# Optimization experiments

Hardware: AMD Instinct MI355X
Metric: run time of the kernel (lower is better)

The kernel has to match this reference:

```python
import jax, jax.numpy as jnp
import numpy as np
from jax import lax

DIM = 64
HEADS = 8
B, H, W = 4, 256, 256


def layer_norm(x, w, b):
    # WithBias LayerNorm over channel dim (dim=1 of NCHW), per-pixel
    mu = jnp.mean(x, axis=1, keepdims=True)
    var = jnp.mean((x - mu) ** 2, axis=1, keepdims=True)
    xn = (x - mu) / jnp.sqrt(var + 1e-5)
    return xn * w[None, :, None, None] + b[None, :, None, None]


def conv1x1(x, w, b=None):
    out = jnp.einsum('oc,bchw->bohw', w, x)
    if b is not None:
        out = out + b[None, :, None, None]
    return out


def dwconv3x3(x, w):
    # w: [C,1,3,3], depthwise (groups=C), stride 1, pad 1
    return lax.conv_general_dilated(
        x, w, window_strides=(1, 1), padding=((1, 1), (1, 1)),
        feature_group_count=x.shape[1],
        dimension_numbers=('NCHW', 'OIHW', 'NCHW'))


def modulation(v, y, mw, mb):
    # mw: [4, C, C] = [scale0, scale1, shift0, shift1]; mb: [4, C]
    s = conv1x1(jax.nn.leaky_relu(conv1x1(y, mw[0], mb[0]), 0.1), mw[1], mb[1])
    t = conv1x1(jax.nn.leaky_relu(conv1x1(y, mw[2], mb[2]), 0.1), mw[3], mb[3])
    return v * (s + 1.0) + t


def _heads(t):
    b, c, h, w = t.shape
    return t.reshape(b, HEADS, c // HEADS, h * w)


def channel_attn(q, k, v, temp):
    b, c, h, w = v.shape
    q, k, v = _heads(q), _heads(k), _heads(v)  # b, head, ch, hw
    q = q / jnp.maximum(jnp.linalg.norm(q, axis=-1, keepdims=True), 1e-12)
    k = k / jnp.maximum(jnp.linalg.norm(k, axis=-1, keepdims=True), 1e-12)
    attn = jnp.einsum('bhcn,bhdn->bhcd', q, k) * temp[None]  # small CxC
    attn = jax.nn.softmax(attn, axis=-1)
    out = jnp.einsum('bhcd,bhdn->bhcn', attn, v)
    return out.reshape(b, c, h, w)


def setup_inputs() -> dict:
    key = jax.random.key(0)
    ks = jax.random.split(key, 24)
    sc = 0.05
    d = {
        'x': jax.random.normal(ks[0], (B, DIM, H, W), jnp.float32),
        'y': jax.random.normal(ks[1], (B, DIM, H, W), jnp.float32),
        'ln_w': jnp.ones((DIM,), jnp.float32),
        'ln_b': jnp.zeros((DIM,), jnp.float32),
        'temp': jnp.ones((HEADS, 1, 1), jnp.float32),
        'kv1_w': jax.random.normal(ks[2], (2 * DIM, DIM), jnp.float32) * sc,
        'kvdw1_w': jax.random.normal(ks[3], (2 * DIM, 1, 3, 3), jnp.float32) * sc,
        'q1_w': jax.random.normal(ks[4], (DIM, DIM), jnp.float32) * sc,
        'qdw1_w': jax.random.normal(ks[5], (DIM, 1, 3, 3), jnp.float32) * sc,
        'po1_w': jax.random.normal(ks[6], (DIM, DIM), jnp.float32) * sc,
        'kv2_w': jax.random.normal(ks[7], (2 * DIM, DIM), jnp.float32) * sc,
        'kvdw2_w': jax.random.normal(ks[8], (2 * DIM, 1, 3, 3), jnp.float32) * sc,
        'q2_w': jax.random.normal(ks[9], (DIM, DIM), jnp.float32) * sc,
        'qdw2_w': jax.random.normal(ks[10], (DIM, 1, 3, 3), jnp.float32) * sc,
        'po2_w': jax.random.normal(ks[11], (DIM, DIM), jnp.float32) * sc,
        'mm1_w': jax.random.normal(ks[12], (4, DIM, DIM), jnp.float32) * sc,
        'mm1_b': jnp.zeros((4, DIM), jnp.float32),
        'mm2_w': jax.random.normal(ks[13], (4, DIM, DIM), jnp.float32) * sc,
        'mm2_b': jnp.zeros((4, DIM), jnp.float32),
    }
    return d


def reference(x, y, ln_w, ln_b, temp,
              kv1_w, kvdw1_w, q1_w, qdw1_w, po1_w,
              kv2_w, kvdw2_w, q2_w, qdw2_w, po2_w,
              mm1_w, mm1_b, mm2_w, mm2_b):
    x1 = layer_norm(x, ln_w, ln_b)
    y1 = layer_norm(y, ln_w, ln_b)  # original reuses self.norm1 for both

    # branch 1: kv from x1, q from y1, v modulated by x, residual y
    kv1 = dwconv3x3(conv1x1(x1, kv1_w), kvdw1_w)
    k1, v1 = jnp.split(kv1, 2, axis=1)
    q1 = dwconv3x3(conv1x1(y1, q1_w), qdw1_w)
    v1 = modulation(v1, x, mm1_w, mm1_b)
    out1 = conv1x1(channel_attn(q1, k1, v1, temp), po1_w) + y

    # branch 2: kv from y1, q from x1, v modulated by y, residual x
    kv2 = dwconv3x3(conv1x1(y1, kv2_w), kvdw2_w)
    k2, v2 = jnp.split(kv2, 2, axis=1)
    q2 = dwconv3x3(conv1x1(x1, q2_w), qdw2_w)
    v2 = modulation(v2, y, mm2_w, mm2_b)
    out2 = conv1x1(channel_attn(q2, k2, v2, temp), po2_w) + x

    return (out1, out2)
```

## Files before the change

### kernel.cpp

```cpp
#include <hip/hip_runtime.h>
#include <hip/hip_bf16.h>

#define HW 65536
#define BATCH 4
#define NPIX (BATCH*HW)

typedef unsigned short u16;
typedef unsigned int   u32;
typedef __attribute__((ext_vector_type(8))) short bh8;
typedef __attribute__((ext_vector_type(4))) float f4;

__device__ __forceinline__ float b2f(u16 u){
    u32 i = ((u32)u) << 16; float f; __builtin_memcpy(&f, &i, 4); return f;
}
__device__ __forceinline__ u16 f2b(float f){
    __hip_bfloat16 h = __float2bfloat16(f); u16 u; __builtin_memcpy(&u, &h, 2); return u;
}

__device__ __forceinline__ f4 mfma16(bh8 a, bh8 b, f4 c){
    return __builtin_amdgcn_mfma_f32_16x16x32_bf16(a, b, c, 0, 0, 0);
}

struct CvtJob { const float* src; u16* dst; int n; const float* cs; };
struct SetupArgs {
    CvtJob j[12];
    const float* kvw[2]; const float* qw[2];
    const float* lnw; const float* lnb;
    float* sums; float* lnc;
};
__global__ __launch_bounds__(256) void setup_kernel(SetupArgs S){
    int blk = blockIdx.x;
    if (blk < 12){
        const CvtJob J = S.j[blk];
        if (J.cs){
            for (int i = threadIdx.x; i < J.n; i += 256) J.dst[i] = f2b(J.src[i] * J.cs[i & 63]);
        } else {
            for (int i = threadIdx.x; i < J.n; i += 256) J.dst[i] = f2b(J.src[i]);
        }
        return;
    }
    int pb = blk - 12;
    if (pb == 0){
        for (int i = threadIdx.x; i < 5120; i += 256) S.sums[i] = 0.f;
    } else {
        int seg = pb - 1;
        int o = threadIdx.x;
        if (o < 192){
            const float* W = (o < 128) ? S.kvw[seg] : S.qw[1-seg];
            int row = (o < 128) ? o : o - 128;
            float a = 0.f, bb = 0.f;
            for (int c = 0; c < 64; c++){
                float wv = W[row*64 + c];
                a = fmaf(wv, S.lnw[c], a); bb = fmaf(wv, S.lnb[c], bb);
            }
            S.lnc[seg*384 + o] = a; S.lnc[seg*384 + 192 + o] = bb;
        }
    }
}

struct GemmMerged {
    const float* in[2];
    const u16* wa[2];
    const float* rs[2]; const float* rb[2];
    u16* out0[2]; u16* out1[2]; u16* out2[2];
};
__global__ __launch_bounds__(256) void gemmln_kernel(GemmMerged G){
    __shared__ u16 wl[192*64];
    int seg = blockIdx.x >> 10, tile = blockIdx.x & 1023;
    int w = threadIdx.x >> 6, lane = threadIdx.x & 63;
    int quad = lane >> 4, l16 = lane & 15;
    int b = tile >> 8;
    int pbase = ((tile & 255) << 8) + (w << 6) + (l16 << 2);

    const float* in = G.in[seg];
    f4 fin[8], fin2[8];
    #pragma unroll
    for (int j = 0; j < 8; j++)
        fin[j] = *(const f4*)(in + ((size_t)b*64 + quad*8 + j)*HW + pbase);
    #pragma unroll
    for (int j = 0; j < 8; j++)
        fin2[j] = *(const f4*)(in + ((size_t)b*64 + 32 + quad*8 + j)*HW + pbase);

    {
        const u16* W = G.wa[seg];
        for (int i = threadIdx.x; i < 192*8; i += 256){
            int row = i >> 3, ch = i & 7;
            uint4 v = *(const uint4*)(W + row*64 + ch*8);
            *(uint4*)(wl + row*64 + ((ch ^ (row & 7)) << 3)) = v;
        }
    }
    __syncthreads();

    float s1[4] = {0.f,0.f,0.f,0.f}, s2[4] = {0.f,0.f,0.f,0.f};
    bh8 bfr[2][4];
    #pragma unroll
    for (int j = 0; j < 8; j++){
        f4 fv = fin[j];
        #pragma unroll
        for (int p = 0; p < 4; p++){
            float v = fv[p];
            s1[p] += v; s2[p] = fmaf(v, v, s2[p]);
            bfr[0][p][j] = (short)f2b(v);
        }
    }
    #pragma unroll
    for (int j = 0; j < 8; j++){
        f4 fv = fin2[j];
        #pragma unroll
        for (int p = 0; p < 4; p++){
            float v = fv[p];
            s1[p] += v; s2[p] = fmaf(v, v, s2[p]);
            bfr[1][p][j] = (short)f2b(v);
        }
    }

    float mu[4], iv[4];
    #pragma unroll
    for (int p = 0; p < 4; p++){
        s1[p] += __shfl_xor(s1[p], 16); s1[p] += __shfl_xor(s1[p], 32);
        s2[p] += __shfl_xor(s2[p], 16); s2[p] += __shfl_xor(s2[p], 32);
        mu[p] = s1[p]*(1.f/64.f);
        iv[p] = rsqrtf(s2[p]*(1.f/64.f) - mu[p]*mu[p] + 1e-5f);
    }

    const float* rs = G.rs[seg]; const float* rb = G.rb[seg];
    u16* o0 = G.out0[seg]; u16* o1 = G.out1[seg]; u16* o2 = G.out2[seg];
    #pragma unroll
    for (int mi = 0; mi < 12; mi++){
        f4 acc[4];
        #pragma unroll
        for (int p = 0; p < 4; p++) acc[p] = (f4){0.f,0.f,0.f,0.f};
        #pragma unroll
        for (int ks = 0; ks < 2; ks++){
            bh8 a;
            __builtin_memcpy(&a, wl + (mi*16 + l16)*64 + ((((ks<<2)+quad) ^ (l16 & 7)) << 3), 16);
            #pragma unroll
            for (int p = 0; p < 4; p++)
                acc[p] = mfma16(a, bfr[ks][p], acc[p]);
        }
        u16* dst = (mi < 4) ? o0 : (mi < 8) ? o1 : o2;
        #pragma unroll
        for (int r = 0; r < 4; r++){
            int o = mi*16 + quad*4 + r;
            size_t pidx = ((size_t)b*64 + (o & 63))*HW + pbase;
            float rsv = rs[o], rbv = rb[o];
            float v0 = iv[0]*(acc[0][r] - mu[0]*rsv) + rbv;
            float v1 = iv[1]*(acc[1][r] - mu[1]*rsv) + rbv;
            float v2 = iv[2]*(acc[2][r] - mu[2]*rsv) + rbv;
            float v3 = iv[3]*(acc[3][r] - mu[3]*rsv) + rbv;
            uint2 st;
            st.x = (u32)f2b(v0) | ((u32)f2b(v1) << 16);
            st.y = (u32)f2b(v2) | ((u32)f2b(v3) << 16);
            *(uint2*)(dst + pidx) = st;
        }
    }
}

struct Dw6 { const u16* in[6]; u16* out[6]; const float* w[6]; int choff[6]; };
__global__ __launch_bounds__(256) void dw6_kernel(Dw6 A){
    int seg = blockIdx.x >> 13;
    int lid = ((blockIdx.x & 8191) << 8) + threadIdx.x;
    const u16* inp = A.in[seg];
    u16* outp      = A.out[seg];
    const float* wd = A.w[seg];
    int choff      = A.choff[seg];
    int bc = lid >> 13;
    int n8 = lid & 8191;
    int h = n8 >> 5, c8 = (n8 & 31) << 3;
    const float* wc = wd + ((size_t)((bc & 63) + choff))*9;
    const u16* p = inp + (size_t)bc*HW;
    float row[3][10];
    #pragma unroll
    for (int r = 0; r < 3; r++){
        int hh = h - 1 + r;
        bool ok = (unsigned)hh < 256u;
        const u16* pr = p + hh*256 + c8;
        if (ok){
            uint4 m = *(const uint4*)pr;
            row[r][1] = b2f((u16)m.x); row[r][2] = b2f((u16)(m.x>>16));
            row[r][3] = b2f((u16)m.y); row[r][4] = b2f((u16)(m.y>>16));
            row[r][5] = b2f((u16)m.z); row[r][6] = b2f((u16)(m.z>>16));
            row[r][7] = b2f((u16)m.w); row[r][8] = b2f((u16)(m.w>>16));
        } else {
            #pragma unroll
            for (int j = 1; j < 9; j++) row[r][j] = 0.f;
        }
        float lft = __shfl_up(row[r][8], 1);
        float rgt = __shfl_down(row[r][1], 1);
        row[r][0] = (c8 > 0)   ? lft : 0.f;
        row[r][9] = (c8 < 248) ? rgt : 0.f;
    }
    float o[8];
    #pragma unroll
    for (int i = 0; i < 8; i++){
        float a = 0.f;
        #pragma unroll
        for (int r = 0; r < 3; r++){
            a = fmaf(wc[r*3+0], row[r][i],   a);
            a = fmaf(wc[r*3+1], row[r][i+1], a);
            a = fmaf(wc[r*3+2], row[r][i+2], a);
        }
        o[i] = a;
    }
    uint4 st;
    st.x = (u32)f2b(o[0]) | ((u32)f2b(o[1])<<16);
    st.y = (u32)f2b(o[2]) | ((u32)f2b(o[3])<<16);
    st.z = (u32)f2b(o[4]) | ((u32)f2b(o[5])<<16);
    st.w = (u32)f2b(o[6]) | ((u32)f2b(o[7])<<16);
    *(uint4*)(outp + (size_t)bc*HW + h*256 + c8) = st;
}

#define NSL 64
struct AttnDual { const u16* q[2]; const u16* k[2]; float* sums; };
__global__ __launch_bounds__(256) void attn_part_kernel(AttnDual AD){
    int seg = blockIdx.x >> 11;
    int blk = blockIdx.x & 2047;
    int sl = blk & (NSL-1);
    int bh = blk >> 6;
    int b = bh >> 3, h = bh & 7;
    const u16* qp = AD.q[seg] + ((size_t)b*64 + h*8)*HW + sl*(HW/NSL);
    const u16* kp = AD.k[seg] + ((size_t)b*64 + h*8)*HW + sl*(HW/NSL);
    float acc[80];
    #pragma unroll
    for (int i = 0; i < 80; i++) acc[i] = 0.f;
    int n0 = threadIdx.x << 2;
    float qv[8][4], kw[8][4];
    #pragma unroll
    for (int i = 0; i < 8; i++){
        uint2 mq = *(const uint2*)(qp + (size_t)i*HW + n0);
        uint2 mk = *(const uint2*)(kp + (size_t)i*HW + n0);
        qv[i][0] = b2f((u16)(mq.x & 0xffffu)); qv[i][1] = b2f((u16)(mq.x >> 16));
        qv[i][2] = b2f((u16)(mq.y & 0xffffu)); qv[i][3] = b2f((u16)(mq.y >> 16));
        kw[i][0] = b2f((u16)(mk.x & 0xffffu)); kw[i][1] = b2f((u16)(mk.x >> 16));
        kw[i][2] = b2f((u16)(mk.y & 0xffffu)); kw[i][3] = b2f((u16)(mk.y >> 16));
    }
    #pragma unroll
    for (int i = 0; i < 8; i++){
        #pragma unroll
        for (int u = 0; u < 4; u++){
            acc[64+i] = fmaf(qv[i][u], qv[i][u], acc[64+i]);
            acc[72+i] = fmaf(kw[i][u], kw[i][u], acc[72+i]);
        }
        #pragma unroll
        for (int j = 0; j < 8; j++)
            #pragma unroll
            for (int u = 0; u < 4; u++)
                acc[i*8+j] = fmaf(qv[i][u], kw[j][u], acc[i*8+j]);
    }
    __shared__ float sred[4][80];
    int lane = threadIdx.x & 63, wv = threadIdx.x >> 6;
    #pragma unroll
    for (int t = 0; t < 80; t++){
        float r = acc[t];
        r += __shfl_down(r, 32); r += __shfl_down(r, 16); r += __shfl_down(r, 8);
        r += __shfl_down(r, 4);  r += __shfl_down(r, 2);  r += __shfl_down(r, 1);
        if (lane == 0) sred[wv][t] = r;
    }
    __syncthreads();
    if (threadIdx.x < 80){
        int t = threadIdx.x;
        atomicAdd(&AD.sums[seg*2560 + bh*80 + t], sred[0][t]+sred[1][t]+sred[2][t]+sred[3][t]);
    }
}

struct WeffDual { const float* sums; const float* temp; const float* po[2]; u16* weff[2]; };
__global__ __launch_bounds__(64) void weff_kernel(WeffDual WD){
    int seg = blockIdx.x >> 2;
    int b = blockIdx.x & 3;
    const float* po = WD.po[seg];
    u16* weff = WD.weff[seg];
    __shared__ float at[8][8][8];
    int t = threadIdx.x;
    {
        int h = t >> 3, i = t & 7;
        const float* f = WD.sums + seg*2560 + (b*8 + h)*80;
        float iq = 1.f / fmaxf(sqrtf(f[64+i]), 1e-12f);
        float tv = WD.temp[h];
        float row[8]; float m = -1e30f;
        #pragma unroll
        for (int j = 0; j < 8; j++){
            float ik = 1.f / fmaxf(sqrtf(f[72+j]), 1e-12f);
            row[j] = f[i*8+j]*iq*ik*tv;
            m = fmaxf(m, row[j]);
        }
        float s = 0.f;
        #pragma unroll
        for (int j = 0; j < 8; j++){ row[j] = expf(row[j]-m); s += row[j]; }
        float rsv = 1.f/s;
        #pragma unroll
        for (int j = 0; j < 8; j++) at[h][i][j] = row[j]*rsv;
    }
    __syncthreads();
    int o = t;
    for (int g = 0; g < 64; g++){
        int h = g >> 3, j = g & 7;
        float wv = 0.f;
        #pragma unroll
        for (int i = 0; i < 8; i++) wv = fmaf(po[o*64 + h*8 + i], at[h][i][j], wv);
        weff[b*4096 + o*64 + g] = f2b(wv);
    }
}

struct ModFinal {
    const float* in[2]; const u16* wa[2]; const u16* wb[2];
    const float* b0[2]; const float* b2[2]; const float* b1[2]; const float* b3[2];
    const u16* wf[2];
    const u16* v[2];
    const float* resid[2];
    float* out[2];
};
__global__ __launch_bounds__(256) void modfinal_kernel(ModFinal M){
    __shared__ u32 lds[128*128];
    int seg = blockIdx.x >> 10, tile = blockIdx.x & 1023;
    int w = threadIdx.x >> 6, lane = threadIdx.x & 63;
    int quad = lane >> 4, l16 = lane & 15;
    int b = tile >> 8;
    int pbase = ((tile & 255) << 8) + (w << 6) + (l16 << 2);
    int pp = ((w << 4) + l16) << 1;

    const float* in = M.in[seg];
    const u16* wa = M.wa[seg];

    f4 fin[8], fin2[8];
    #pragma unroll
    for (int j = 0; j < 8; j++)
        fin[j] = *(const f4*)(in + ((size_t)b*64 + quad*8 + j)*HW + pbase);
    #pragma unroll
    for (int j = 0; j < 8; j++)
        fin2[j] = *(const f4*)(in + ((size_t)b*64 + 32 + quad*8 + j)*HW + pbase);

    f4 acc[8][4];
    #pragma unroll
    for (int mi = 0; mi < 8; mi++)
        #pragma unroll
        for (int p = 0; p < 4; p++) acc[mi][p] = (f4){0.f,0.f,0.f,0.f};

    #pragma unroll
    for (int ks = 0; ks < 2; ks++){
        bh8 bfr[4];
        #pragma unroll
        for (int j = 0; j < 8; j++){
            f4 fv = (ks == 0) ? fin[j] : fin2[j];
            #pragma unroll
            for (int p = 0; p < 4; p++) bfr[p][j] = (short)f2b(fv[p]);
        }
        #pragma unroll
        for (int mi = 0; mi < 8; mi++){
            bh8 a;
            __builtin_memcpy(&a, wa + (mi*16 + l16)*64 + ks*32 + quad*8, 16);
            #pragma unroll
            for (int p = 0; p < 4; p++)
                acc[mi][p] = mfma16(a, bfr[p], acc[mi][p]);
        }
    }

    uint2 vpref[16];
    {
        const u16* vP = M.v[seg];
        #pragma unroll
        for (int mi = 0; mi < 4; mi++)
        #pragma unroll
        for (int r = 0; r < 4; r++)
            vpref[mi*4+r] = *(const uint2*)(vP + ((size_t)b*64 + mi*16 + quad*4 + r)*HW + pbase);
    }

    {
        const float* b0v = M.b0[seg]; const float* b2v = M.b2[seg];
        #pragma unroll
        for (int mi = 0; mi < 8; mi++)
        #pragma unroll
        for (int r = 0; r < 4; r++){
            int o = mi*16 + quad*4 + r;
            float bi = (o < 64) ? b0v[o] : b2v[o-64];
            float v0 = acc[mi][0][r] + bi; v0 = v0 > 0.f ? v0 : 0.1f*v0;
            float v1 = acc[mi][1][r] + bi; v1 = v1 > 0.f ? v1 : 0.1f*v1;
            float v2 = acc[mi][2][r] + bi; v2 = v2 > 0.f ? v2 : 0.1f*v2;
            float v3 = acc[mi][3][r] + bi; v3 = v3 > 0.f ? v3 : 0.1f*v3;
            uint2 st;
            st.x = (u32)f2b(v0) | ((u32)f2b(v1) << 16);
            st.y = (u32)f2b(v2) | ((u32)f2b(v3) << 16);
            *(uint2*)&lds[o*128 + ((pp + ((o>>2)&3)*8) & 127)] = st;
        }
    }
    __syncthreads();

    const u16* wb = M.wb[seg];
    f4 acc2[8][4];
    #pragma unroll
    for (int mi = 0; mi < 8; mi++)
        #pragma unroll
        for (int p = 0; p < 4; p++) acc2[mi][p] = (f4){0.f,0.f,0.f,0.f};
    #pragma unroll
    for (int ks = 0; ks < 4; ks++){
        int kb = ks*32 + quad*8;
        bh8 bfr[4];
        #pragma unroll
        for (int j = 0; j < 8; j++){
            int ch = kb + j;
            uint2 m = *(const uint2*)&lds[ch*128 + ((pp + ((ch>>2)&3)*8) & 127)];
            bfr[0][j] = (short)(m.x & 0xffffu);
            bfr[1][j] = (short)(m.x >> 16);
            bfr[2][j] = (short)(m.y & 0xffffu);
            bfr[3][j] = (short)(m.y >> 16);
        }
        #pragma unroll
        for (int mi = 0; mi < 8; mi++){
            if (mi < 4 ? (ks < 2) : (ks >= 2)){
                int ksl = (mi >= 4) ? ks - 2 : ks;
                bh8 a;
                __builtin_memcpy(&a, wb + (mi*16 + l16)*64 + ksl*32 + quad*8, 16);
                #pragma unroll
                for (int p = 0; p < 4; p++)
                    acc2[mi][p] = mfma16(a, bfr[p], acc2[mi][p]);
            }
        }
    }
    __syncthreads();

    {
        const float* b1v = M.b1[seg]; const float* b3v = M.b3[seg];
        #pragma unroll
        for (int mi = 0; mi < 4; mi++)
        #pragma unroll
        for (int r = 0; r < 4; r++){
            int o = mi*16 + quad*4 + r;
            uint2 vv = vpref[mi*4+r];
            float va[4] = { b2f((u16)(vv.x & 0xffffu)), b2f((u16)(vv.x >> 16)),
                            b2f((u16)(vv.y & 0xffffu)), b2f((u16)(vv.y >> 16)) };
            float ov[4];
            #pragma unroll
            for (int p = 0; p < 4; p++){
                float s = acc2[mi][p][r] + b1v[o];
                float t = acc2[mi+4][p][r] + b3v[o];
                ov[p] = va[p]*(s+1.f)+t;
            }
            uint2 st;
            st.x = (u32)f2b(ov[0]) | ((u32)f2b(ov[1]) << 16);
            st.y = (u32)f2b(ov[2]) | ((u32)f2b(ov[3]) << 16);
            *(uint2*)&lds[o*128 + ((pp + ((o>>2)&3)*8) & 127)] = st;
        }
    }
    f4 rpre[16];
    {
        const float* resid = M.resid[seg];
        #pragma unroll
        for (int mi = 0; mi < 4; mi++)
        #pragma unroll
        for (int r = 0; r < 4; r++)
            rpre[mi*4+r] = *(const f4*)(resid + ((size_t)b*64 + mi*16 + quad*4 + r)*HW + pbase);
    }
    __syncthreads();

    const u16* wf = M.wf[seg] + b*4096;
    f4 accF[4][4];
    #pragma unroll
    for (int mi = 0; mi < 4; mi++)
        #pragma unroll
        for (int p = 0; p < 4; p++) accF[mi][p] = (f4){0.f,0.f,0.f,0.f};
    #pragma unroll
    for (int ks = 0; ks < 2; ks++){
        int kb = ks*32 + quad*8;
        bh8 bfr[4];
        #pragma unroll
        for (int j = 0; j < 8; j++){
            int ch = kb + j;
            uint2 m = *(const uint2*)&lds[ch*128 + ((pp + ((ch>>2)&3)*8) & 127)];
            bfr[0][j] = (short)(m.x & 0xffffu);
            bfr[1][j] = (short)(m.x >> 16);
            bfr[2][j] = (short)(m.y & 0xffffu);
            bfr[3][j] = (short)(m.y >> 16);
        }
        #pragma unroll
        for (int mi = 0; mi < 4; mi++){
            bh8 a;
            __builtin_memcpy(&a, wf + (mi*16 + l16)*64 + ks*32 + quad*8, 16);
            #pragma unroll
            for (int p = 0; p < 4; p++)
                accF[mi][p] = mfma16(a, bfr[p], accF[mi][p]);
        }
    }
    {
        float* outF = M.out[seg];
        #pragma unroll
        for (int mi = 0; mi < 4; mi++)
        #pragma unroll
        for (int r = 0; r < 4; r++){
            int o = mi*16 + quad*4 + r;
            size_t pidx = ((size_t)b*64 + o)*HW + pbase;
            f4 rr = rpre[mi*4+r];
            f4 st;
            #pragma unroll
            for (int p = 0; p < 4; p++) st[p] = accF[mi][p][r] + rr[p];
            *(f4*)(outF + pidx) = st;
        }
    }
}

extern "C" void kernel_launch(void* const* d_in, const int* in_sizes, int n_in,
                              void* d_out, int out_size, void* d_ws, size_t ws_size,
                              hipStream_t stream){
    const float* x    = (const float*)d_in[0];
    const float* y    = (const float*)d_in[1];
    const float* ln_w = (const float*)d_in[2];
    const float* ln_b = (const float*)d_in[3];
    const float* temp = (const float*)d_in[4];
    const float* kv_w[2]   = {(const float*)d_in[5],  (const float*)d_in[10]};
    const float* kvdw_w[2] = {(const float*)d_in[6],  (const float*)d_in[11]};
    const float* q_w[2]    = {(const float*)d_in[7],  (const float*)d_in[12]};
    const float* qdw_w[2]  = {(const float*)d_in[8],  (const float*)d_in[13]};
    const float* po_w[2]   = {(const float*)d_in[9],  (const float*)d_in[14]};
    const float* mm_w[2]   = {(const float*)d_in[15], (const float*)d_in[17]};
    const float* mm_b[2]   = {(const float*)d_in[16], (const float*)d_in[18]};

    const size_t HPE = (size_t)BATCH*64*HW;
    u16* PL = (u16*)d_ws;
    u16* P[12];
    for (int i = 0; i < 12; i++) P[i] = PL + (size_t)i*HPE;
    float* sums = (float*)(PL + 12*HPE);
    float* lnc  = sums + 5120;
    u16* warena = (u16*)(lnc + 768);
    const int WG[2] = {0, 12288};
    const int WMA[2] = {24576, 40960}, WMB[2] = {32768, 49152};
    const int WEFF[2] = {57344, 73728};

    size_t need = 12*HPE*2 + (5120+768)*4 + 90112*2;
    if (ws_size < need) return;

    SetupArgs S{};
    int nj = 0;
    auto add = [&](const float* s, u16* d, int n, const float* cs){ S.j[nj] = {s, d, n, cs}; nj++; };
    add(kv_w[0], warena + WG[0],        8192, ln_w);
    add(q_w[1],  warena + WG[0] + 8192, 4096, ln_w);
    add(kv_w[1], warena + WG[1],        8192, ln_w);
    add(q_w[0],  warena + WG[1] + 8192, 4096, ln_w);
    for (int br = 0; br < 2; br++){
        add(mm_w[br],        warena + WMA[br],        4096, nullptr);
        add(mm_w[br]+8192,   warena + WMA[br] + 4096, 4096, nullptr);
        add(mm_w[br]+4096,   warena + WMB[br],        4096, nullptr);
        add(mm_w[br]+12288,  warena + WMB[br] + 4096, 4096, nullptr);
    }
    S.kvw[0] = kv_w[0]; S.kvw[1] = kv_w[1];
    S.qw[0]  = q_w[0];  S.qw[1]  = q_w[1];
    S.lnw = ln_w; S.lnb = ln_b; S.sums = sums; S.lnc = lnc;
    setup_kernel<<<15, 256, 0, stream>>>(S);

    const int GT = NPIX/256;

    GemmMerged GK{};
    GK.in[0] = x; GK.in[1] = y;
    GK.wa[0] = warena + WG[0]; GK.wa[1] = warena + WG[1];
    GK.rs[0] = lnc;        GK.rb[0] = lnc + 192;
    GK.rs[1] = lnc + 384;  GK.rb[1] = lnc + 576;
    GK.out0[0] = P[0]; GK.out1[0] = P[1]; GK.out2[0] = P[5];
    GK.out0[1] = P[2]; GK.out1[1] = P[3]; GK.out2[1] = P[4];
    gemmln_kernel<<<2*GT, 256, 0, stream>>>(GK);

    Dw6 D{};
    D.in[0] = P[0];  D.out[0] = P[6];  D.w[0] = kvdw_w[0]; D.choff[0] = 0;
    D.in[1] = P[1];  D.out[1] = P[7];  D.w[1] = kvdw_w[0]; D.choff[1] = 64;
    D.in[2] = P[4];  D.out[2] = P[8];  D.w[2] = qdw_w[0];  D.choff[2] = 0;
    D.in[3] = P[2];  D.out[3] = P[9];  D.w[3] = kvdw_w[1]; D.choff[3] = 0;
    D.in[4] = P[3];  D.out[4] = P[10]; D.w[4] = kvdw_w[1]; D.choff[4] = 64;
    D.in[5] = P[5];  D.out[5] = P[11]; D.w[5] = qdw_w[1];  D.choff[5] = 0;
    dw6_kernel<<<6*8192, 256, 0, stream>>>(D);

    AttnDual AD{};
    AD.q[0] = P[8];  AD.k[0] = P[6];
    AD.q[1] = P[11]; AD.k[1] = P[9];
    AD.sums = sums;
    attn_part_kernel<<<2*BATCH*8*NSL, 256, 0, stream>>>(AD);

    WeffDual WD{};
    WD.sums = sums; WD.temp = temp;
    WD.po[0] = po_w[0]; WD.po[1] = po_w[1];
    WD.weff[0] = warena + WEFF[0]; WD.weff[1] = warena + WEFF[1];
    weff_kernel<<<2*BATCH, 64, 0, stream>>>(WD);

    float* outp = (float*)d_out;
    ModFinal M{};
    M.in[0] = x; M.in[1] = y;
    M.wa[0] = warena + WMA[0]; M.wa[1] = warena + WMA[1];
    M.wb[0] = warena + WMB[0]; M.wb[1] = warena + WMB[1];
    M.b0[0] = mm_b[0];       M.b0[1] = mm_b[1];
    M.b2[0] = mm_b[0] + 128; M.b2[1] = mm_b[1] + 128;
    M.b1[0] = mm_b[0] + 64;  M.b1[1] = mm_b[1] + 64;
    M.b3[0] = mm_b[0] + 192; M.b3[1] = mm_b[1] + 192;
    M.wf[0] = warena + WEFF[0]; M.wf[1] = warena + WEFF[1];
    M.v[0] = P[7]; M.v[1] = P[10];
    M.resid[0] = y; M.resid[1] = x;
    M.out[0] = outp; M.out[1] = outp + HPE;
    modfinal_kernel<<<2*GT, 256, 0, stream>>>(M);
}
```

Before: 611.7 us.

## Restructure modulation kernel to halve LDS and cut register pressure for occupancy

The modulation+final kernel is reordered to process the scale and shift MLP branches one after the other, each through a 64-channel LDS staging area, instead of holding all 128 hidden channels in accumulators and LDS at once. LDS per block drops from 64KB to 32KB and launch bounds request 4 blocks per CU, so more waves can be resident to hide global memory latency. The price is extra LDS round-trips and barriers, the intermediate scale values are now kept packed as bf16 in registers, and capping registers may cause spills.

```diff
diff --git a/kernel.cpp b/kernel.cpp
--- a/kernel.cpp
+++ b/kernel.cpp
@@ -309,8 +309,8 @@
     const float* resid[2];
     float* out[2];
 };
-__global__ __launch_bounds__(256) void modfinal_kernel(ModFinal M){
-    __shared__ u32 lds[128*128];
+__global__ __launch_bounds__(256,4) void modfinal_kernel(ModFinal M){
+    __shared__ u32 lds[64*128];
     int seg = blockIdx.x >> 10, tile = blockIdx.x & 1023;
     int w = threadIdx.x >> 6, lane = threadIdx.x & 63;
     int quad = lane >> 4, l16 = lane & 15;
@@ -320,178 +320,241 @@
 
     const float* in = M.in[seg];
     const u16* wa = M.wa[seg];
-
-    f4 fin[8], fin2[8];
-    #pragma unroll
-    for (int j = 0; j < 8; j++)
-        fin[j] = *(const f4*)(in + ((size_t)b*64 + quad*8 + j)*HW + pbase);
-    #pragma unroll
-    for (int j = 0; j < 8; j++)
-        fin2[j] = *(const f4*)(in + ((size_t)b*64 + 32 + quad*8 + j)*HW + pbase);
-
-    f4 acc[8][4];
-    #pragma unroll
-    for (int mi = 0; mi < 8; mi++)
-        #pragma unroll
-        for (int p = 0; p < 4; p++) acc[mi][p] = (f4){0.f,0.f,0.f,0.f};
-
+    const u16* wb = M.wb[seg];
+
+    bh8 bfr[2][4];
+    {
+        f4 fin[8];
+        #pragma unroll
+        for (int j = 0; j < 8; j++)
+            fin[j] = *(const f4*)(in + ((size_t)b*64 + quad*8 + j)*HW + pbase);
+        #pragma unroll
+        for (int j = 0; j < 8; j++)
+            #pragma unroll
+            for (int p = 0; p < 4; p++) bfr[0][p][j] = (short)f2b(fin[j][p]);
+        #pragma unroll
+        for (int j = 0; j < 8; j++)
+            fin[j] = *(const f4*)(in + ((size_t)b*64 + 32 + quad*8 + j)*HW + pbase);
+        #pragma unroll
+        for (int j = 0; j < 8; j++)
+            #pragma unroll
+            for (int p = 0; p < 4; p++) bfr[1][p][j] = (short)f2b(fin[j][p]);
+    }
+
+    {
+        const float* b0v = M.b0[seg];
+        #pragma unroll
+        for (int mi = 0; mi < 4; mi++){
+            f4 acc[4];
+            #pragma unroll
+            for (int p = 0; p < 4; p++) acc[p] = (f4){0.f,0.f,0.f,0.f};
+            #pragma unroll
+            for (int ks = 0; ks < 2; ks++){
+                bh8 a;
+                __builtin_memcpy(&a, wa + (mi*16 + l16)*64 + ks*32 + quad*8, 16);
+                #pragma unroll
+                for (int p = 0; p < 4; p++) acc[p] = mfma16(a, bfr[ks][p], acc[p]);
+            }
+            #pragma unroll
+            for (int r = 0; r < 4; r++){
+                int o = mi*16 + quad*4 + r;
+                float bi = b0v[o];
+                float v0 = acc[0][r] + bi; v0 = v0 > 0.f ? v0 : 0.1f*v0;
+                float v1 = acc[1][r] + bi; v1 = v1 > 0.f ? v1 : 0.1f*v1;
+                float v2 = acc[2][r] + bi; v2 = v2 > 0.f ? v2 : 0.1f*v2;
+                float v3 = acc[3][r] + bi; v3 = v3 > 0.f ? v3 : 0.1f*v3;
+                uint2 st;
+                st.x = (u32)f2b(v0) | ((u32)f2b(v1) << 16);
+                st.y = (u32)f2b(v2) | ((u32)f2b(v3) << 16);
+                *(uint2*)&lds[o*128 + ((pp + ((o>>2)&3)*8) & 127)] = st;
+            }
+        }
+    }
+    __syncthreads();
+
+    bh8 bsr[2][4];
     #pragma unroll
     for (int ks = 0; ks < 2; ks++){
-        bh8 bfr[4];
-        #pragma unroll
-        for (int j = 0; j < 8; j++){
-            f4 fv = (ks == 0) ? fin[j] : fin2[j];
-            #pragma unroll
-            for (int p = 0; p < 4; p++) bfr[p][j] = (short)f2b(fv[p]);
-        }
-        #pragma unroll
-        for (int mi = 0; mi < 8; mi++){
-            bh8 a;
-            __builtin_memcpy(&a, wa + (mi*16 + l16)*64 + ks*32 + quad*8, 16);
-            #pragma unroll
-            for (int p = 0; p < 4; p++)
-                acc[mi][p] = mfma16(a, bfr[p], acc[mi][p]);
-        }
-    }
-
-    uint2 vpref[16];
-    {
-        const u16* vP = M.v[seg];
-        #pragma unroll
-        for (int mi = 0; mi < 4; mi++)
-        #pragma unroll
-        for (int r = 0; r < 4; r++)
-            vpref[mi*4+r] = *(const uint2*)(vP + ((size_t)b*64 + mi*16 + quad*4 + r)*HW + pbase);
-    }
-
-    {
-        const float* b0v = M.b0[seg]; const float* b2v = M.b2[seg];
-        #pragma unroll
-        for (int mi = 0; mi < 8; mi++)
-        #pragma unroll
-        for (int r = 0; r < 4; r++){
-            int o = mi*16 + quad*4 + r;
-            float bi = (o < 64) ? b0v[o] : b2v[o-64];
-            float v0 = acc[mi][0][r] + bi; v0 = v0 > 0.f ? v0 : 0.1f*v0;
-            float v1 = acc[mi][1][r] + bi; v1 = v1 > 0.f ? v1 : 0.1f*v1;
-            float v2 = acc[mi][2][r] + bi; v2 = v2 > 0.f ? v2 : 0.1f*v2;
-            float v3 = acc[mi][3][r] + bi; v3 = v3 > 0.f ? v3 : 0.1f*v3;
-            uint2 st;
-            st.x = (u32)f2b(v0) | ((u32)f2b(v1) << 16);
-            st.y = (u32)f2b(v2) | ((u32)f2b(v3) << 16);
-            *(uint2*)&lds[o*128 + ((pp + ((o>>2)&3)*8) & 127)] = st;
-        }
-    }
-    __syncthreads();
-
-    const u16* wb = M.wb[seg];
-    f4 acc2[8][4];
-    #pragma unroll
-    for (int mi = 0; mi < 8; mi++)
-        #pragma unroll
-        for (int p = 0; p < 4; p++) acc2[mi][p] = (f4){0.f,0.f,0.f,0.f};
-    #pragma unroll
-    for (int ks = 0; ks < 4; ks++){
         int kb = ks*32 + quad*8;
-        bh8 bfr[4];
         #pragma unroll
         for (int j = 0; j < 8; j++){
             int ch = kb + j;
             uint2 m = *(const uint2*)&lds[ch*128 + ((pp + ((ch>>2)&3)*8) & 127)];
-            bfr[0][j] = (short)(m.x & 0xffffu);
-            bfr[1][j] = (short)(m.x >> 16);
-            bfr[2][j] = (short)(m.y & 0xffffu);
-            bfr[3][j] = (short)(m.y >> 16);
-        }
-        #pragma unroll
-        for (int mi = 0; mi < 8; mi++){
-            if (mi < 4 ? (ks < 2) : (ks >= 2)){
-                int ksl = (mi >= 4) ? ks - 2 : ks;
+            bsr[ks][0][j] = (short)(m.x & 0xffffu);
+            bsr[ks][1][j] = (short)(m.x >> 16);
+            bsr[ks][2][j] = (short)(m.y & 0xffffu);
+            bsr[ks][3][j] = (short)(m.y >> 16);
+        }
+    }
+    __syncthreads();
+
+    {
+        const float* b2v = M.b2[seg];
+        #pragma unroll
+        for (int mi = 0; mi < 4; mi++){
+            f4 acc[4];
+            #pragma unroll
+            for (int p = 0; p < 4; p++) acc[p] = (f4){0.f,0.f,0.f,0.f};
+            #pragma unroll
+            for (int ks = 0; ks < 2; ks++){
                 bh8 a;
-                __builtin_memcpy(&a, wb + (mi*16 + l16)*64 + ksl*32 + quad*8, 16);
+                __builtin_memcpy(&a, wa + ((64 + mi*16 + l16))*64 + ks*32 + quad*8, 16);
                 #pragma unroll
-                for (int p = 0; p < 4; p++)
-                    acc2[mi][p] = mfma16(a, bfr[p], acc2[mi][p]);
-            }
-        }
-    }
-    __syncthreads();
-
-    {
-        const float* b1v = M.b1[seg]; const float* b3v = M.b3[seg];
-        #pragma unroll
-        for (int mi = 0; mi < 4; mi++)
-        #pragma unroll
-        for (int r = 0; r < 4; r++){
-            int o = mi*16 + quad*4 + r;
-            uint2 vv = vpref[mi*4+r];
-            float va[4] = { b2f((u16)(vv.x & 0xffffu)), b2f((u16)(vv.x >> 16)),
-                            b2f((u16)(vv.y & 0xffffu)), b2f((u16)(vv.y >> 16)) };
-            float ov[4];
-            #pragma unroll
-            for (int p = 0; p < 4; p++){
-                float s = acc2[mi][p][r] + b1v[o];
-                float t = acc2[mi+4][p][r] + b3v[o];
-                ov[p] = va[p]*(s+1.f)+t;
-            }
-            uint2 st;
-            st.x = (u32)f2b(ov[0]) | ((u32)f2b(ov[1]) << 16);
-            st.y = (u32)f2b(ov[2]) | ((u32)f2b(ov[3]) << 16);
-            *(uint2*)&lds[o*128 + ((pp + ((o>>2)&3)*8) & 127)] = st;
-        }
-    }
-    f4 rpre[16];
-    {
-        const float* resid = M.resid[seg];
-        #pragma unroll
-        for (int mi = 0; mi < 4; mi++)
-        #pragma unroll
-        for (int r = 0; r < 4; r++)
-            rpre[mi*4+r] = *(const f4*)(resid + ((size_t)b*64 + mi*16 + quad*4 + r)*HW + pbase);
-    }
-    __syncthreads();
-
-    const u16* wf = M.wf[seg] + b*4096;
-    f4 accF[4][4];
-    #pragma unroll
-    for (int mi = 0; mi < 4; mi++)
-        #pragma unroll
-        for (int p = 0; p < 4; p++) accF[mi][p] = (f4){0.f,0.f,0.f,0.f};
+                for (int p = 0; p < 4; p++) acc[p] = mfma16(a, bfr[ks][p], acc[p]);
+            }
+            #pragma unroll
+            for (int r = 0; r < 4; r++){
+                int o = mi*16 + quad*4 + r;
+                float bi = b2v[o];
+                float v0 = acc[0][r] + bi; v0 = v0 > 0.f ? v0 : 0.1f*v0;
+                float v1 = acc[1][r] + bi; v1 = v1 > 0.f ? v1 : 0.1f*v1;
+                float v2 = acc[2][r] + bi; v2 = v2 > 0.f ? v2 : 0.1f*v2;
+                float v3 = acc[3][r] + bi; v3 = v3 > 0.f ? v3 : 0.1f*v3;
+                uint2 st;
+                st.x = (u32)f2b(v0) | ((u32)f2b(v1) << 16);
+                st.y = (u32)f2b(v2) | ((u32)f2b(v3) << 16);
+                *(uint2*)&lds[o*128 + ((pp + ((o>>2)&3)*8) & 127)] = st;
+            }
+        }
+    }
+
+    uint2 spk[4][4];
+    {
+        const float* b1v = M.b1[seg];
+        #pragma unroll
+        for (int mi = 0; mi < 4; mi++){
+            f4 acc[4];
+            #pragma unroll
+            for (int p = 0; p < 4; p++) acc[p] = (f4){0.f,0.f,0.f,0.f};
+            #pragma unroll
+            for (int ks = 0; ks < 2; ks++){
+                bh8 a;
+                __builtin_memcpy(&a, wb + (mi*16 + l16)*64 + ks*32 + quad*8, 16);
+                #pragma unroll
+                for (int p = 0; p < 4; p++) acc[p] = mfma16(a, bsr[ks][p], acc[p]);
+            }
+            #pragma unroll
+            for (int r = 0; r < 4; r++){
+                int o = mi*16 + quad*4 + r;
+                float bi = b1v[o];
+                uint2 st;
+                st.x = (u32)f2b(acc[0][r] + bi) | ((u32)f2b(acc[1][r] + bi) << 16);
+                st.y = (u32)f2b(acc[2][r] + bi) | ((u32)f2b(acc[3][r] + bi) << 16);
+                spk[mi][r] = st;
+            }
+        }
+    }
+    __syncthreads();
+
+    bh8 btr[2][4];
     #pragma unroll
     for (int ks = 0; ks < 2; ks++){
         int kb = ks*32 + quad*8;
-        bh8 bfr[4];
         #pragma unroll
         for (int j = 0; j < 8; j++){
             int ch = kb + j;
             uint2 m = *(const uint2*)&lds[ch*128 + ((pp + ((ch>>2)&3)*8) & 127)];
-            bfr[0][j] = (short)(m.x & 0xffffu);
-            bfr[1][j] = (short)(m.x >> 16);
-            bfr[2][j] = (short)(m.y & 0xffffu);
-            bfr[3][j] = (short)(m.y >> 16);
-        }
+            btr[ks][0][j] = (short)(m.x & 0xffffu);
+            btr[ks][1][j] = (short)(m.x >> 16);
+            btr[ks][2][j] = (short)(m.y & 0xffffu);
+            btr[ks][3][j] = (short)(m.y >> 16);
+        }
+    }
+    uint2 vpref[16];
+    {
+        const u16* vP = M.v[seg];
+        #pragma unroll
+        for (int mi = 0; mi < 4; mi++)
+        #pragma unroll
+        for (int r = 0; r < 4; r++)
+            vpref[mi*4+r] = *(const uint2*)(vP + ((size_t)b*64 + mi*16 + quad*4 + r)*HW + pbase);
+    }
+    __syncthreads();
+
+    {
+        const float* b3v = M.b3[seg];
         #pragma unroll
         for (int mi = 0; mi < 4; mi++){
-            bh8 a;
-            __builtin_memcpy(&a, wf + (mi*16 + l16)*64 + ks*32 + quad*8, 16);
-            #pragma unroll
-            for (int p = 0; p < 4; p++)
-                accF[mi][p] = mfma16(a, bfr[p], accF[mi][p]);
-        }
-    }
-    {
+            f4 acc[4];
+            #pragma unroll
+            for (int p = 0; p < 4; p++) acc[p] = (f4){0.f,0.f,0.f,0.f};
+            #pragma unroll
+            for (int ks = 0; ks < 2; ks++){
+                bh8 a;
+                __builtin_memcpy(&a, wb + ((64 + mi*16 + l16))*64 + ks*32 + quad*8, 16);
+                #pragma unroll
+                for (int p = 0; p < 4; p++) acc[p] = mfma16(a, btr[ks][p], acc[p]);
+            }
+            #pragma unroll
+            for (int r = 0; r < 4; r++){
+                int o = mi*16 + quad*4 + r;
+                float bi = b3v[o];
+                uint2 sv = spk[mi][r];
+                uint2 vv = vpref[mi*4+r];
+                float s0 = b2f((u16)(sv.x & 0xffffu)), s1 = b2f((u16)(sv.x >> 16));
+                float s2 = b2f((u16)(sv.y & 0xffffu)), s3 = b2f((u16)(sv.y >> 16));
+                float va0 = b2f((u16)(vv.x & 0xffffu)), va1 = b2f((u16)(vv.x >> 16));
+                float va2 = b2f((u16)(vv.y & 0xffffu)), va3 = b2f((u16)(vv.y >> 16));
+                float o0 = va0*(s0+1.f) + (acc[0][r] + bi);
+                float o1 = va1*(s1+1.f) + (acc[1][r] + bi);
+                float o2 = va2*(s2+1.f) + (acc[2][r] + bi);
+                float o3 = va3*(s3+1.f) + (acc[3][r] + bi);
+                uint2 st;
+                st.x = (u32)f2b(o0) | ((u32)f2b(o1) << 16);
+                st.y = (u32)f2b(o2) | ((u32)f2b(o3) << 16);
+                *(uint2*)&lds[o*128 + ((pp + ((o>>2)&3)*8) & 127)] = st;
+            }
+        }
+    }
+    __syncthreads();
+
+    {
+        const float* resid = M.resid[seg];
         float* outF = M.out[seg];
+        const u16* wf = M.wf[seg] + b*4096;
+        f4 rpre[16];
         #pragma unroll
         for (int mi = 0; mi < 4; mi++)
         #pragma unroll
-        for (int r = 0; r < 4; r++){
-            int o = mi*16 + quad*4 + r;
-            size_t pidx = ((size_t)b*64 + o)*HW + pbase;
-            f4 rr = rpre[mi*4+r];
-            f4 st;
-            #pragma unroll
-            for (int p = 0; p < 4; p++) st[p] = accF[mi][p][r] + rr[p];
-            *(f4*)(outF + pidx) = st;
+        for (int r = 0; r < 4; r++)
+            rpre[mi*4+r] = *(const f4*)(resid + ((size_t)b*64 + mi*16 + quad*4 + r)*HW + pbase);
+
+        bh8 b3r[2][4];
+        #pragma unroll
+        for (int ks = 0; ks < 2; ks++){
+            int kb = ks*32 + quad*8;
+            #pragma unroll
+            for (int j = 0; j < 8; j++){
+                int ch = kb + j;
+                uint2 m = *(const uint2*)&lds[ch*128 + ((pp + ((ch>>2)&3)*8) & 127)];
+                b3r[ks][0][j] = (short)(m.x & 0xffffu);
+                b3r[ks][1][j] = (short)(m.x >> 16);
+                b3r[ks][2][j] = (short)(m.y & 0xffffu);
+                b3r[ks][3][j] = (short)(m.y >> 16);
+            }
+        }
+        #pragma unroll
+        for (int mi = 0; mi < 4; mi++){
+            f4 acc[4];
+            #pragma unroll
+            for (int p = 0; p < 4; p++) acc[p] = (f4){0.f,0.f,0.f,0.f};
+            #pragma unroll
+            for (int ks = 0; ks < 2; ks++){
+                bh8 a;
+                __builtin_memcpy(&a, wf + (mi*16 + l16)*64 + ks*32 + quad*8, 16);
+                #pragma unroll
+                for (int p = 0; p < 4; p++) acc[p] = mfma16(a, b3r[ks][p], acc[p]);
+            }
+            #pragma unroll
+            for (int r = 0; r < 4; r++){
+                int o = mi*16 + quad*4 + r;
+                size_t pidx = ((size_t)b*64 + o)*HW + pbase;
+                f4 rr = rpre[mi*4+r];
+                f4 st;
+                #pragma unroll
+                for (int p = 0; p < 4; p++) st[p] = acc[p][r] + rr[p];
+                *(f4*)(outF + pidx) = st;
+            }
         }
     }
 }
```

Measured after the change: 631.3 us. +3.2%, slower.

## Coalesce LN-GEMM input loads via LDS transpose, read weights from global

Applied to the files above, without the earlier changes.

The gemmln kernel now loads each input channel row with contiguous per-thread float4 reads, converts to bf16 and stages them in a swizzled LDS tile. Per-pixel LayerNorm partial sums are reduced through shared memory instead of wave shuffles. Weight fragments are read directly from global (cache-resident) memory instead of being staged in LDS. Launch bounds request 4 blocks per CU. This aims to improve global load coalescing and occupancy, at the cost of an extra LDS round trip and uncached-in-LDS weight reads.

```diff
diff --git a/kernel.cpp b/kernel.cpp
--- a/kernel.cpp
+++ b/kernel.cpp
@@ -64,65 +64,73 @@
     const float* rs[2]; const float* rb[2];
     u16* out0[2]; u16* out1[2]; u16* out2[2];
 };
-__global__ __launch_bounds__(256) void gemmln_kernel(GemmMerged G){
-    __shared__ u16 wl[192*64];
+__global__ __launch_bounds__(256,4) void gemmln_kernel(GemmMerged G){
+    __shared__ u32 ti[64*128];
+    __shared__ float ts[8*256];
     int seg = blockIdx.x >> 10, tile = blockIdx.x & 1023;
+    int b = tile >> 8;
+    int PB = (tile & 255) << 8;
+
+    const float* in = G.in[seg] + (size_t)b*64*HW + PB;
+
+    {
+        int ct = threadIdx.x >> 6, pt = threadIdx.x & 63;
+        f4 fin[16];
+        #pragma unroll
+        for (int c8 = 0; c8 < 16; c8++)
+            fin[c8] = *(const f4*)(in + (size_t)(c8*4 + ct)*HW + pt*4);
+        float s1p[4] = {0.f,0.f,0.f,0.f}, s2p[4] = {0.f,0.f,0.f,0.f};
+        #pragma unroll
+        for (int c8 = 0; c8 < 16; c8++){
+            int ch = c8*4 + ct;
+            f4 fv = fin[c8];
+            uint2 st;
+            st.x = (u32)f2b(fv[0]) | ((u32)f2b(fv[1]) << 16);
+            st.y = (u32)f2b(fv[2]) | ((u32)f2b(fv[3]) << 16);
+            *(uint2*)&ti[ch*128 + ((2*pt + ((ch>>2)&3)*8) & 127)] = st;
+            #pragma unroll
+            for (int p = 0; p < 4; p++){
+                s1p[p] += fv[p];
+                s2p[p] = fmaf(fv[p], fv[p], s2p[p]);
+            }
+        }
+        #pragma unroll
+        for (int p = 0; p < 4; p++){
+            ts[(0*4 + ct)*256 + pt*4 + p] = s1p[p];
+            ts[(1*4 + ct)*256 + pt*4 + p] = s2p[p];
+        }
+    }
+    __syncthreads();
+
     int w = threadIdx.x >> 6, lane = threadIdx.x & 63;
     int quad = lane >> 4, l16 = lane & 15;
-    int b = tile >> 8;
-    int pbase = ((tile & 255) << 8) + (w << 6) + (l16 << 2);
-
-    const float* in = G.in[seg];
-    f4 fin[8], fin2[8];
-    #pragma unroll
-    for (int j = 0; j < 8; j++)
-        fin[j] = *(const f4*)(in + ((size_t)b*64 + quad*8 + j)*HW + pbase);
-    #pragma unroll
-    for (int j = 0; j < 8; j++)
-        fin2[j] = *(const f4*)(in + ((size_t)b*64 + 32 + quad*8 + j)*HW + pbase);
-
-    {
-        const u16* W = G.wa[seg];
-        for (int i = threadIdx.x; i < 192*8; i += 256){
-            int row = i >> 3, ch = i & 7;
-            uint4 v = *(const uint4*)(W + row*64 + ch*8);
-            *(uint4*)(wl + row*64 + ((ch ^ (row & 7)) << 3)) = v;
-        }
-    }
-    __syncthreads();
-
-    float s1[4] = {0.f,0.f,0.f,0.f}, s2[4] = {0.f,0.f,0.f,0.f};
+    int gp = w*16 + l16;
+    int pbase = PB + gp*4;
+
     bh8 bfr[2][4];
     #pragma unroll
-    for (int j = 0; j < 8; j++){
-        f4 fv = fin[j];
-        #pragma unroll
-        for (int p = 0; p < 4; p++){
-            float v = fv[p];
-            s1[p] += v; s2[p] = fmaf(v, v, s2[p]);
-            bfr[0][p][j] = (short)f2b(v);
-        }
-    }
-    #pragma unroll
-    for (int j = 0; j < 8; j++){
-        f4 fv = fin2[j];
-        #pragma unroll
-        for (int p = 0; p < 4; p++){
-            float v = fv[p];
-            s1[p] += v; s2[p] = fmaf(v, v, s2[p]);
-            bfr[1][p][j] = (short)f2b(v);
-        }
-    }
-
+    for (int ks = 0; ks < 2; ks++){
+        #pragma unroll
+        for (int j = 0; j < 8; j++){
+            int ch = ks*32 + quad*8 + j;
+            uint2 m = *(const uint2*)&ti[ch*128 + ((2*gp + ((ch>>2)&3)*8) & 127)];
+            bfr[ks][0][j] = (short)(m.x & 0xffffu);
+            bfr[ks][1][j] = (short)(m.x >> 16);
+            bfr[ks][2][j] = (short)(m.y & 0xffffu);
+            bfr[ks][3][j] = (short)(m.y >> 16);
+        }
+    }
     float mu[4], iv[4];
     #pragma unroll
     for (int p = 0; p < 4; p++){
-        s1[p] += __shfl_xor(s1[p], 16); s1[p] += __shfl_xor(s1[p], 32);
-        s2[p] += __shfl_xor(s2[p], 16); s2[p] += __shfl_xor(s2[p], 32);
-        mu[p] = s1[p]*(1.f/64.f);
-        iv[p] = rsqrtf(s2[p]*(1.f/64.f) - mu[p]*mu[p] + 1e-5f);
-    }
-
+        int px = gp*4 + p;
+        float s1 = ts[0*256 + px] + ts[1*256 + px] + ts[2*256 + px] + ts[3*256 + px];
+        float s2 = ts[(4+0)*256 + px] + ts[(4+1)*256 + px] + ts[(4+2)*256 + px] + ts[(4+3)*256 + px];
+        mu[p] = s1*(1.f/64.f);
+        iv[p] = rsqrtf(s2*(1.f/64.f) - mu[p]*mu[p] + 1e-5f);
+    }
+
+    const u16* W = G.wa[seg];
     const float* rs = G.rs[seg]; const float* rb = G.rb[seg];
     u16* o0 = G.out0[seg]; u16* o1 = G.out1[seg]; u16* o2 = G.out2[seg];
     #pragma unroll
@@ -133,7 +141,7 @@
         #pragma unroll
         for (int ks = 0; ks < 2; ks++){
             bh8 a;
-            __builtin_memcpy(&a, wl + (mi*16 + l16)*64 + ((((ks<<2)+quad) ^ (l16 & 7)) << 3), 16);
+            __builtin_memcpy(&a, W + (mi*16 + l16)*64 + ks*32 + quad*8, 16);
             #pragma unroll
             for (int p = 0; p < 4; p++)
                 acc[p] = mfma16(a, bfr[ks][p], acc[p]);
```

Measured after the change: 618.2 us. About the same (+1.1%).
